# Kernel tuning notes

Measured on AMD Instinct MI355X. Metric: run time of the kernel, lower is better.

The kernel has to match this reference:

```python
import jax, jax.numpy as jnp
import numpy as np

D_MODEL, D_FFN, N_LEVELS, N_HEADS, N_POINTS = 256, 1024, 4, 8, 4
B, LQ = 2, 8192
SHAPES = [(128, 128), (64, 64), (32, 32), (16, 16)]  # (H_l, W_l) per level
D_HEAD = D_MODEL // N_HEADS


def setup_inputs() -> dict:
    key = jax.random.key(0)
    ks = jax.random.split(key, 16)
    S = sum(h * w for h, w in SHAPES)

    def lin_w(k, fin, fout):
        s = 1.0 / np.sqrt(fin)
        return jax.random.uniform(k, (fin, fout), jnp.float32, -s, s)

    inp = {
        "tgt": jax.random.normal(ks[0], (B, LQ, D_MODEL), jnp.float32),
        "query_pos": jax.random.normal(ks[1], (B, LQ, D_MODEL), jnp.float32),
        "reference_points": jax.random.uniform(ks[2], (B, LQ, N_LEVELS, 2), jnp.float32),
        "src": jax.random.normal(ks[3], (B, S, D_MODEL), jnp.float32),
        "spatial_shapes": np.array(SHAPES, dtype=np.int64),
        "level_start_index": np.concatenate([[0], np.cumsum([h * w for h, w in SHAPES])[:-1]]).astype(np.int64),
        "W_value": lin_w(ks[4], D_MODEL, D_MODEL),
        "b_value": jnp.zeros((D_MODEL,), jnp.float32),
        "W_off": lin_w(ks[5], D_MODEL, N_HEADS * N_LEVELS * N_POINTS * 2),
        "b_off": 0.5 * jax.random.normal(ks[6], (N_HEADS * N_LEVELS * N_POINTS * 2,), jnp.float32),
        "W_attn": lin_w(ks[7], D_MODEL, N_HEADS * N_LEVELS * N_POINTS),
        "b_attn": jnp.zeros((N_HEADS * N_LEVELS * N_POINTS,), jnp.float32),
        "W_out": lin_w(ks[8], D_MODEL, D_MODEL),
        "b_out": jnp.zeros((D_MODEL,), jnp.float32),
        "ln1_g": jnp.ones((D_MODEL,), jnp.float32),
        "ln1_b": jnp.zeros((D_MODEL,), jnp.float32),
        "W1": lin_w(ks[9], D_MODEL, D_FFN),
        "b1": jnp.zeros((D_FFN,), jnp.float32),
        "W2": lin_w(ks[10], D_FFN, D_MODEL),
        "b2": jnp.zeros((D_MODEL,), jnp.float32),
        "ln3_g": jnp.ones((D_MODEL,), jnp.float32),
        "ln3_b": jnp.zeros((D_MODEL,), jnp.float32),
    }
    return inp


def _layer_norm(x, g, b, eps=1e-5):
    mu = jnp.mean(x, -1, keepdims=True)
    var = jnp.mean((x - mu) ** 2, -1, keepdims=True)
    return (x - mu) * jax.lax.rsqrt(var + eps) * g + b


def _ms_deform_attn(q, reference_points, src, shapes,
                    W_value, b_value, W_off, b_off, W_attn, b_attn, W_out, b_out):
    Bq, Lq, _ = q.shape
    value = (src @ W_value + b_value).reshape(Bq, -1, N_HEADS, D_HEAD)
    value = jnp.transpose(value, (0, 2, 1, 3))  # [B, H, S, Dh]
    off = (q @ W_off + b_off).reshape(Bq, Lq, N_HEADS, N_LEVELS, N_POINTS, 2)
    attn = jax.nn.softmax((q @ W_attn + b_attn).reshape(Bq, Lq, N_HEADS, N_LEVELS * N_POINTS), axis=-1)
    attn = attn.reshape(Bq, Lq, N_HEADS, N_LEVELS, N_POINTS)
    # offset normalizer is (W_l, H_l) per level
    normalizer = jnp.array([[w, h] for h, w in shapes], jnp.float32)
    loc = reference_points[:, :, None, :, None, :] + off / normalizer[None, None, None, :, None, :]

    out = jnp.zeros((Bq, Lq, N_HEADS, D_HEAD), jnp.float32)
    start = 0
    for l, (Hl, Wl) in enumerate(shapes):
        Nl = Hl * Wl
        v_l = value[:, :, start:start + Nl]  # [B, H, Nl, Dh]
        start += Nl
        loc_l = jnp.transpose(loc[:, :, :, l, :, :], (0, 2, 1, 3, 4))  # [B, H, Lq, P, 2]
        # grid_sample (align_corners=False, zero padding) pixel coords
        x = loc_l[..., 0] * Wl - 0.5
        y = loc_l[..., 1] * Hl - 0.5
        x0, y0 = jnp.floor(x), jnp.floor(y)
        wx, wy = x - x0, y - y0
        acc = jnp.zeros((Bq, N_HEADS, Lq, N_POINTS, D_HEAD), jnp.float32)
        for dx, dy, w in ((0, 0, (1 - wx) * (1 - wy)), (1, 0, wx * (1 - wy)),
                          (0, 1, (1 - wx) * wy), (1, 1, wx * wy)):
            xi, yi = x0 + dx, y0 + dy
            valid = (xi >= 0) & (xi < Wl) & (yi >= 0) & (yi < Hl)
            idx = (jnp.clip(yi, 0, Hl - 1) * Wl + jnp.clip(xi, 0, Wl - 1)).astype(jnp.int32)
            g = jnp.take_along_axis(v_l, idx.reshape(Bq, N_HEADS, -1, 1), axis=2)
            g = g.reshape(Bq, N_HEADS, Lq, N_POINTS, D_HEAD)
            acc = acc + jnp.where(valid[..., None], w[..., None] * g, 0.0)
        a = jnp.transpose(attn[:, :, :, l, :], (0, 2, 1, 3))  # [B, H, Lq, P]
        out = out + jnp.einsum('bhqp,bhqpd->bqhd', a, acc)
    return out.reshape(Bq, Lq, D_MODEL) @ W_out + b_out


def reference(tgt, query_pos, reference_points, src, spatial_shapes, level_start_index,
              W_value, b_value, W_off, b_off, W_attn, b_attn, W_out, b_out,
              ln1_g, ln1_b, W1, b1, W2, b2, ln3_g, ln3_b):
    shapes = [(int(h), int(w)) for h, w in np.asarray(spatial_shapes)]
    q = tgt + query_pos  # with_pos_embed
    tgt2 = _ms_deform_attn(q, reference_points, src, shapes,
                           W_value, b_value, W_off, b_off, W_attn, b_attn, W_out, b_out)
    x = _layer_norm(tgt + tgt2, ln1_g, ln1_b)  # dropout = identity (eval)
    ff = jax.nn.relu(x @ W1 + b1) @ W2 + b2
    return _layer_norm(x + ff, ln3_g, ln3_b)
```

## Files before the change

### kernel.cpp

```cpp
#include <hip/hip_runtime.h>
#include <hip/hip_bf16.h>
#include <hip/hip_fp16.h>
#include <math.h>

#define D_MODEL   256
#define D_FFN     1024
#define N_LEVELS  4
#define N_HEADS   8
#define N_POINTS  4
#define BATCH     2
#define LQ        8192
#define S_TOTAL   21760
#define M_Q       (BATCH*LQ)
#define M_V       (BATCH*S_TOTAL)
#define VTILES    (M_V/128)

typedef __attribute__((ext_vector_type(8))) short bf16x8;
typedef __attribute__((ext_vector_type(4))) float floatx4;

struct alignas(8)  bh4 { __hip_bfloat16 a, b, c, d; };
struct alignas(16) bh8 { __hip_bfloat16 v[8]; };

__device__ __forceinline__ void gld_lds16(const void* g, void* l) {
    __builtin_amdgcn_global_load_lds(
        (const __attribute__((address_space(1))) void*)g,
        (__attribute__((address_space(3))) void*)l, 16, 0, 0);
}

template<int BM, int BN, int K>
__device__ __forceinline__ void gemm_core(const __hip_bfloat16* __restrict__ A,
                                          const __hip_bfloat16* __restrict__ Bt,
                                          int row0, int nb0, int lda, int ldb,
                                          short* As, short* Bs,
                                          floatx4 (&acc)[BM/64][BN/16])
{
    constexpr int NT  = BN / 16;
    constexpr int AF  = BM / 64;
    constexpr int BCH = BN / 64;
    constexpr int NIT = K / 32;

    const int tid  = threadIdx.x;
    const int w    = tid >> 6;
    const int lane = tid & 63;
    const int quad = lane >> 4;
    const int l15  = lane & 15;
    const size_t ldaB = (size_t)lda * 2, ldbB = (size_t)ldb * 2;

    const char* gA[AF]; int lA[AF];
#pragma unroll
    for (int i = 0; i < AF; i++) {
        int o = (w * AF + i) * 1024 + lane * 16;
        gA[i] = (const char*)A + (size_t)(row0 + (o >> 6)) * ldaB + (o & 63);
        lA[i] = (w * AF + i) * 512;
    }
    const char* gB[BCH]; int lB[BCH];
#pragma unroll
    for (int j = 0; j < BCH; j++) {
        int o = (w * BCH + j) * 1024 + lane * 16;
        gB[j] = (const char*)Bt + (size_t)(nb0 + (o >> 6)) * ldbB + (o & 63);
        lB[j] = (w * BCH + j) * 512;
    }

#pragma unroll
    for (int i = 0; i < AF; i++)  gld_lds16(gA[i], &As[lA[i]]);
#pragma unroll
    for (int j = 0; j < BCH; j++) gld_lds16(gB[j], &Bs[lB[j]]);

#pragma unroll 8
    for (int it = 0; it < NIT; ++it) {
        __syncthreads();
        const int cb = it & 1;
        if (it + 1 < NIT) {
            const size_t kb = (size_t)(it + 1) * 64;
            const int nb = cb ^ 1;
#pragma unroll
            for (int i = 0; i < AF; i++)  gld_lds16(gA[i] + kb, &As[nb * BM * 32 + lA[i]]);
#pragma unroll
            for (int j = 0; j < BCH; j++) gld_lds16(gB[j] + kb, &Bs[nb * BN * 32 + lB[j]]);
        }
        const short* Ab = &As[cb * BM * 32];
        const short* Bb = &Bs[cb * BN * 32];
        bf16x8 af[AF];
#pragma unroll
        for (int mi = 0; mi < AF; mi++)
            af[mi] = *(const bf16x8*)&Ab[(w * (AF * 16) + mi * 16 + l15) * 32 + quad * 8];
#pragma unroll
        for (int ni = 0; ni < NT; ni++) {
            bf16x8 bfr = *(const bf16x8*)&Bb[(ni * 16 + l15) * 32 + quad * 8];
#pragma unroll
            for (int mi = 0; mi < AF; mi++)
                acc[mi][ni] = __builtin_amdgcn_mfma_f32_16x16x32_bf16(af[mi], bfr, acc[mi][ni], 0, 0, 0);
        }
    }
}

template<int BM, int BN, int K, int EPI>
__global__ __launch_bounds__(256)
void mfma_gemm(const __hip_bfloat16* __restrict__ A,
               const __hip_bfloat16* __restrict__ Bt,
               const float* __restrict__ bias,
               float* __restrict__ outf, __hip_bfloat16* __restrict__ outb,
               int lda, int ldb, int ldOut, long zStride)
{
    constexpr int NT = BN / 16, AF = BM / 64;
    __shared__ alignas(16) short As[2 * BM * 32];
    __shared__ alignas(16) short Bs[2 * BN * 32];

    const int tid = threadIdx.x, w = tid >> 6, lane = tid & 63;
    const int quad = lane >> 4, l15 = lane & 15;
    const int row0 = blockIdx.x * BM, nb0 = blockIdx.y * BN;
    const int z = blockIdx.z;

    floatx4 acc[AF][NT];
#pragma unroll
    for (int mi = 0; mi < AF; mi++)
#pragma unroll
        for (int ni = 0; ni < NT; ni++) acc[mi][ni] = (floatx4){0.f, 0.f, 0.f, 0.f};

    gemm_core<BM, BN, K>(A + (size_t)z * K, Bt + (size_t)z * K,
                         row0, nb0, lda, ldb, As, Bs, acc);

    float bias_c[NT];
#pragma unroll
    for (int ni = 0; ni < NT; ni++) bias_c[ni] = bias ? bias[nb0 + ni * 16 + l15] : 0.f;

    float* of = outf + (size_t)z * zStride;
#pragma unroll
    for (int mi = 0; mi < AF; mi++)
#pragma unroll
        for (int r = 0; r < 4; r++) {
            int row = row0 + w * (AF * 16) + mi * 16 + quad * 4 + r;
            size_t rb = (size_t)row * ldOut + nb0;
#pragma unroll
            for (int ni = 0; ni < NT; ni++) {
                float v = acc[mi][ni][r] + bias_c[ni];
                if (EPI == 2) outb[rb + ni * 16 + l15] = __float2bfloat16(fmaxf(v, 0.f));
                else          of[rb + ni * 16 + l15] = v;
            }
        }
}

__global__ __launch_bounds__(256)
void mfma_gemm_vq(const __hip_bfloat16* __restrict__ srcb,
                  const __hip_bfloat16* __restrict__ Wvt,
                  const float* __restrict__ b_value,
                  __hip_bfloat16* __restrict__ valueb,
                  const __hip_bfloat16* __restrict__ qb,
                  const __hip_bfloat16* __restrict__ Woat,
                  const float* __restrict__ b_off, const float* __restrict__ b_attn,
                  float* __restrict__ offb, float* __restrict__ attnb)
{
    __shared__ alignas(16) short As[2 * 128 * 32];
    __shared__ alignas(16) short Bs[2 * 128 * 32];

    const bool isV = blockIdx.x < VTILES;
    if (isV && blockIdx.y == 2) return;

    const int tid = threadIdx.x, w = tid >> 6, lane = tid & 63;
    const int quad = lane >> 4, l15 = lane & 15;
    const int nb0 = blockIdx.y * 128;

    floatx4 acc[2][8];
#pragma unroll
    for (int mi = 0; mi < 2; mi++)
#pragma unroll
        for (int ni = 0; ni < 8; ni++) acc[mi][ni] = (floatx4){0.f, 0.f, 0.f, 0.f};

    if (isV) {
        const int row0 = blockIdx.x * 128;
        gemm_core<128, 128, 256>(srcb, Wvt, row0, nb0, 256, 256, As, Bs, acc);
        float bias_c[8];
#pragma unroll
        for (int ni = 0; ni < 8; ni++) bias_c[ni] = b_value[nb0 + ni * 16 + l15];
#pragma unroll
        for (int mi = 0; mi < 2; mi++)
#pragma unroll
            for (int r = 0; r < 4; r++) {
                int row = row0 + w * 32 + mi * 16 + quad * 4 + r;
                size_t rb = (size_t)row * 256 + nb0;
#pragma unroll
                for (int ni = 0; ni < 8; ni++)
                    valueb[rb + ni * 16 + l15] = __float2bfloat16(acc[mi][ni][r] + bias_c[ni]);
            }
        return;
    }

    const int row0 = (blockIdx.x - VTILES) * 128;
    gemm_core<128, 128, 256>(qb, Woat, row0, nb0, 256, 256, As, Bs, acc);

    if (blockIdx.y < 2) {
        float bias_c[8];
#pragma unroll
        for (int ni = 0; ni < 8; ni++) bias_c[ni] = b_off[nb0 + ni * 16 + l15];
#pragma unroll
        for (int mi = 0; mi < 2; mi++)
#pragma unroll
            for (int r = 0; r < 4; r++) {
                int row = row0 + w * 32 + mi * 16 + quad * 4 + r;
                size_t rb = (size_t)row * 256 + nb0;
#pragma unroll
                for (int ni = 0; ni < 8; ni++)
                    offb[rb + ni * 16 + l15] = acc[mi][ni][r] + bias_c[ni];
            }
    } else {
        float bias_c[8];
#pragma unroll
        for (int ni = 0; ni < 8; ni++) bias_c[ni] = b_attn[ni * 16 + l15];
#pragma unroll
        for (int mi = 0; mi < 2; mi++)
#pragma unroll
            for (int r = 0; r < 4; r++) {
                int row = row0 + w * 32 + mi * 16 + quad * 4 + r;
                size_t rb = (size_t)row * 128;
#pragma unroll
                for (int ni = 0; ni < 8; ni++) {
                    float v = acc[mi][ni][r] + bias_c[ni];
                    float m = v;
#pragma unroll
                    for (int msk = 1; msk <= 8; msk <<= 1) m = fmaxf(m, __shfl_xor(m, msk));
                    float e = __expf(v - m);
                    float ssum = e;
#pragma unroll
                    for (int msk = 1; msk <= 8; msk <<= 1) ssum += __shfl_xor(ssum, msk);
                    attnb[rb + ni * 16 + l15] = e / ssum;
                }
            }
    }
}

__global__ __launch_bounds__(256)
void ln_kernel(const float* __restrict__ in1, const float* __restrict__ in2,
               const float* __restrict__ resid, const float* __restrict__ bias,
               const float* __restrict__ g, const float* __restrict__ b,
               float* __restrict__ outf, __hip_bfloat16* __restrict__ outb)
{
    const int row  = blockIdx.x * 4 + (threadIdx.x >> 6);
    const int lane = threadIdx.x & 63;
    const size_t rb = (size_t)row * 256 + lane * 4;

    float4 v = *(const float4*)(resid + rb);
    float4 a = *(const float4*)(in1 + rb);
    v.x += a.x; v.y += a.y; v.z += a.z; v.w += a.w;
    if (in2) {
        float4 c = *(const float4*)(in2 + rb);
        v.x += c.x; v.y += c.y; v.z += c.z; v.w += c.w;
    }
    if (bias) {
        float4 c = *(const float4*)(bias + lane * 4);
        v.x += c.x; v.y += c.y; v.z += c.z; v.w += c.w;
    }
    float s  = v.x + v.y + v.z + v.w;
    float sq = v.x * v.x + v.y * v.y + v.z * v.z + v.w * v.w;
#pragma unroll
    for (int msk = 1; msk <= 32; msk <<= 1) {
        s += __shfl_xor(s, msk); sq += __shfl_xor(sq, msk);
    }
    float mean = s * (1.f / 256.f);
    float var  = sq * (1.f / 256.f) - mean * mean;
    float rstd = rsqrtf(var + 1e-5f);
    float4 gg = *(const float4*)(g + lane * 4);
    float4 bb = *(const float4*)(b + lane * 4);
    float4 o;
    o.x = (v.x - mean) * rstd * gg.x + bb.x;
    o.y = (v.y - mean) * rstd * gg.y + bb.y;
    o.z = (v.z - mean) * rstd * gg.z + bb.z;
    o.w = (v.w - mean) * rstd * gg.w + bb.w;
    *(float4*)(outf + rb) = o;
    if (outb)
        *(bh4*)(outb + rb) = { __float2bfloat16(o.x), __float2bfloat16(o.y),
                               __float2bfloat16(o.z), __float2bfloat16(o.w) };
}

__global__ __launch_bounds__(256)
void prep_kernel(const float* w0, const float* w1, const float* w2,
                 const float* w3, const float* w4, const float* w5,
                 __hip_bfloat16* o0, __hip_bfloat16* o1, __hip_bfloat16* o2,
                 __hip_bfloat16* o3, __hip_bfloat16* o4, __hip_bfloat16* o5,
                 const float* src, __hip_bfloat16* srcb,
                 const float* tgt, const float* qpos, __hip_bfloat16* qb)
{
    const int bx = blockIdx.x;
    if (bx < 736) {
        int t = bx;
        const float* s; __hip_bfloat16* dst; int Kd, Nd, tl;
        if      (t < 64)  { s = w0; dst = o0; Kd = 256;  Nd = 256;  tl = t; }
        else if (t < 128) { s = w1; dst = o1; Kd = 256;  Nd = 256;  tl = t - 64; }
        else if (t < 160) { s = w2; dst = o2; Kd = 256;  Nd = 128;  tl = t - 128; }
        else if (t < 224) { s = w3; dst = o3; Kd = 256;  Nd = 256;  tl = t - 160; }
        else if (t < 480) { s = w4; dst = o4; Kd = 256;  Nd = 1024; tl = t - 224; }
        else              { s = w5; dst = o5; Kd = 1024; Nd = 256;  tl = t - 480; }
        int ntn = Nd >> 5;
        int kt = tl / ntn, nt = tl - kt * ntn;
        __shared__ float T[32][33];
        int tx = threadIdx.x & 31, ty = threadIdx.x >> 5;
#pragma unroll
        for (int i = 0; i < 4; i++) {
            int k = kt * 32 + ty + i * 8;
            T[tx][ty + i * 8] = s[(size_t)k * Nd + nt * 32 + tx];
        }
        __syncthreads();
#pragma unroll
        for (int i = 0; i < 4; i++) {
            int n = nt * 32 + ty + i * 8;
            dst[(size_t)n * Kd + kt * 32 + tx] = __float2bfloat16(T[ty + i * 8][tx]);
        }
    } else if (bx < 736 + 10880) {
        int i = (bx - 736) * 256 + threadIdx.x;
        float4 v = ((const float4*)src)[i];
        ((bh4*)srcb)[i] = { __float2bfloat16(v.x), __float2bfloat16(v.y),
                            __float2bfloat16(v.z), __float2bfloat16(v.w) };
    } else {
        int i = (bx - 736 - 10880) * 256 + threadIdx.x;
        float4 x = ((const float4*)tgt)[i];
        float4 y = ((const float4*)qpos)[i];
        ((bh4*)qb)[i] = { __float2bfloat16(x.x + y.x), __float2bfloat16(x.y + y.y),
                          __float2bfloat16(x.z + y.z), __float2bfloat16(x.w + y.w) };
    }
}

#define QB 8
__global__ __launch_bounds__(256)
void sample_kernel(const float* __restrict__ refp, const float* __restrict__ offb,
                   const float* __restrict__ attn,
                   const __hip_bfloat16* __restrict__ value,
                   __hip_bfloat16* __restrict__ tgt2)
{
    __shared__ unsigned spk[64 * 65];

    const int q0  = blockIdx.x * QB;
    const int tid = threadIdx.x;

#pragma unroll
    for (int k = 0; k < 4; k++) {
        const int it = tid + k * 256;
        const int ql = it >> 7, h = (it >> 4) & 7, lp = it & 15;
        const int l = lp >> 2, p = lp & 3;
        const int q = q0 + ql, b = q >> 13;
        const int Wl = 128 >> l;
        const int LST = (l == 0) ? 0 : (l == 1) ? 16384 : (l == 2) ? 20480 : 21504;

        const float rx = refp[((size_t)q * N_LEVELS + l) * 2 + 0];
        const float ry = refp[((size_t)q * N_LEVELS + l) * 2 + 1];
        const float ox = offb[(size_t)q * 256 + h * 32 + l * 8 + p * 2 + 0];
        const float oy = offb[(size_t)q * 256 + h * 32 + l * 8 + p * 2 + 1];
        const float a  = attn[(size_t)q * 128 + h * 16 + lp];

        const float x = rx * Wl - 0.5f + ox;
        const float y = ry * Wl - 0.5f + oy;
        const float x0f = floorf(x), y0f = floorf(y);
        const float wx = x - x0f, wy = y - y0f;
        const int ix = (int)x0f, iy = (int)y0f;
        const int base = b * S_TOTAL + LST;
        const int g = ql * 8 + h;
        const float cw[4] = {(1.f - wx) * (1.f - wy) * a, wx * (1.f - wy) * a,
                             (1.f - wx) * wy * a,         wx * wy * a};
#pragma unroll
        for (int c = 0; c < 4; c++) {
            const int xi = ix + (c & 1), yi = iy + (c >> 1);
            const bool valid = ((unsigned)xi < (unsigned)Wl) && ((unsigned)yi < (unsigned)Wl);
            const unsigned pix = valid ? (unsigned)(base + yi * Wl + xi) : (unsigned)base;
            const __half hw = __float2half(valid ? cw[c] : 0.f);
            spk[(lp * 4 + c) * 65 + g] = (pix << 16) | (unsigned)__half_as_ushort(hw);
        }
    }
    __syncthreads();

    const int ql = tid >> 5, h = (tid >> 2) & 7, d4 = tid & 3;
    const int q = q0 + ql, g = ql * 8 + h;
    const int c0 = h * 32 + d4 * 8;
    const char* vb = (const char*)value + (size_t)c0 * 2;

    float ac[8] = {0.f, 0.f, 0.f, 0.f, 0.f, 0.f, 0.f, 0.f};
#pragma unroll
    for (int sc = 0; sc < 64; sc++) {
        unsigned u = spk[sc * 65 + g];
        float wv = __half2float(__ushort_as_half((unsigned short)(u & 0xffffu)));
        uint4 rv = *(const uint4*)(vb + ((size_t)(u >> 16) << 9));
        ac[0] += wv * __uint_as_float(rv.x << 16);
        ac[1] += wv * __uint_as_float(rv.x & 0xffff0000u);
        ac[2] += wv * __uint_as_float(rv.y << 16);
        ac[3] += wv * __uint_as_float(rv.y & 0xffff0000u);
        ac[4] += wv * __uint_as_float(rv.z << 16);
        ac[5] += wv * __uint_as_float(rv.z & 0xffff0000u);
        ac[6] += wv * __uint_as_float(rv.w << 16);
        ac[7] += wv * __uint_as_float(rv.w & 0xffff0000u);
    }
    bh8 o;
#pragma unroll
    for (int i = 0; i < 8; i++) o.v[i] = __float2bfloat16(ac[i]);
    *(bh8*)(tgt2 + (size_t)q * 256 + c0) = o;
}

extern "C" void kernel_launch(void* const* d_in, const int* in_sizes, int n_in,
                              void* d_out, int out_size, void* d_ws, size_t ws_size,
                              hipStream_t stream) {
    const float* tgt     = (const float*)d_in[0];
    const float* qpos    = (const float*)d_in[1];
    const float* refp    = (const float*)d_in[2];
    const float* src     = (const float*)d_in[3];
    const float* W_value = (const float*)d_in[6];
    const float* b_value = (const float*)d_in[7];
    const float* W_off   = (const float*)d_in[8];
    const float* b_off   = (const float*)d_in[9];
    const float* W_attn  = (const float*)d_in[10];
    const float* b_attn  = (const float*)d_in[11];
    const float* W_out   = (const float*)d_in[12];
    const float* b_out   = (const float*)d_in[13];
    const float* ln1_g   = (const float*)d_in[14];
    const float* ln1_b   = (const float*)d_in[15];
    const float* W1      = (const float*)d_in[16];
    const float* b1      = (const float*)d_in[17];
    const float* W2      = (const float*)d_in[18];
    const float* b2      = (const float*)d_in[19];
    const float* ln3_g   = (const float*)d_in[20];
    const float* ln3_b   = (const float*)d_in[21];
    float* out = (float*)d_out;

    char* p = (char*)d_ws;
    auto nxt = [&](size_t b) { char* r = p; p += (b + 255) & ~(size_t)255; return r; };
    __hip_bfloat16* Wvt    = (__hip_bfloat16*)nxt((size_t)256 * 256 * 2);
    __hip_bfloat16* Woat   = (__hip_bfloat16*)nxt((size_t)384 * 256 * 2);
    __hip_bfloat16* Woutt  = (__hip_bfloat16*)nxt((size_t)256 * 256 * 2);
    __hip_bfloat16* W1t    = (__hip_bfloat16*)nxt((size_t)1024 * 256 * 2);
    __hip_bfloat16* W2t    = (__hip_bfloat16*)nxt((size_t)256 * 1024 * 2);
    __hip_bfloat16* srcb   = (__hip_bfloat16*)nxt((size_t)M_V * 256 * 2);
    __hip_bfloat16* qb     = (__hip_bfloat16*)nxt((size_t)M_Q * 256 * 2);
    __hip_bfloat16* valueb = (__hip_bfloat16*)nxt((size_t)M_V * 256 * 2);
    float*          offb   = (float*)nxt((size_t)M_Q * 256 * 4);
    float*          attnb  = (float*)nxt((size_t)M_Q * 128 * 4);
    __hip_bfloat16* tgt2b  = (__hip_bfloat16*)nxt((size_t)M_Q * 256 * 2);
    float*          x      = (float*)nxt((size_t)M_Q * 256 * 4);
    __hip_bfloat16* xb     = (__hip_bfloat16*)nxt((size_t)M_Q * 256 * 2);
    __hip_bfloat16* hb     = (__hip_bfloat16*)nxt((size_t)M_Q * 1024 * 2);
    float* t2o = offb;
    float* p0  = (float*)srcb;
    float* p1  = p0 + (size_t)M_Q * 256;

    dim3 blk(256);

    prep_kernel<<<dim3(736 + 10880 + 4096), blk, 0, stream>>>(
        W_value, W_off, W_attn, W_out, W1, W2,
        Wvt, Woat, Woat + 256 * 256, Woutt, W1t, W2t,
        src, srcb, tgt, qpos, qb);

    mfma_gemm_vq<<<dim3(VTILES + M_Q / 128, 3), blk, 0, stream>>>(
        srcb, Wvt, b_value, valueb, qb, Woat, b_off, b_attn, offb, attnb);

    sample_kernel<<<dim3(M_Q / QB), blk, 0, stream>>>(refp, offb, attnb, valueb, tgt2b);

    mfma_gemm<64, 128, 256, 0><<<dim3(M_Q / 64, 2), blk, 0, stream>>>(
        tgt2b, Woutt, b_out, t2o, nullptr, 256, 256, 256, 0);

    ln_kernel<<<dim3(M_Q / 4), blk, 0, stream>>>(
        t2o, nullptr, tgt, nullptr, ln1_g, ln1_b, x, xb);

    mfma_gemm<128, 128, 256, 2><<<dim3(M_Q / 128, 8), blk, 0, stream>>>(
        xb, W1t, b1, nullptr, hb, 256, 256, 1024, 0);

    mfma_gemm<64, 128, 512, 0><<<dim3(M_Q / 64, 2, 2), blk, 0, stream>>>(
        hb, W2t, nullptr, p0, nullptr, 1024, 1024, 256, (long)M_Q * 256);

    ln_kernel<<<dim3(M_Q / 4), blk, 0, stream>>>(
        p0, p1, x, b2, ln3_g, ln3_b, out, nullptr);
}
```

Baseline: 301.2 us.

## Fuse fp32-to-bf16 input conversion into value/query GEMM and batch sample gathers

The separate conversion pass over src and tgt+query_pos is removed. The value/offset GEMM now loads fp32 A tiles directly, adds query_pos in registers, packs to bf16 and writes them into LDS, which avoids a full write and re-read of the bf16 copies. The output projection now stores bf16 that the first layernorm reads, and the sampling loop issues 16 gathers at a time with an occupancy hint to raise memory-level parallelism. In exchange, A tiles are staged through registers rather than async global-to-LDS loads, and the output projection result is rounded to bf16 before the residual add.

```diff
diff --git a/kernel.cpp b/kernel.cpp
--- a/kernel.cpp
+++ b/kernel.cpp
@@ -27,6 +27,15 @@
         (__attribute__((address_space(3))) void*)l, 16, 0, 0);
 }
 
+__device__ __forceinline__ bh8 pack8(float4 a, float4 b) {
+    bh8 o;
+    o.v[0] = __float2bfloat16(a.x); o.v[1] = __float2bfloat16(a.y);
+    o.v[2] = __float2bfloat16(a.z); o.v[3] = __float2bfloat16(a.w);
+    o.v[4] = __float2bfloat16(b.x); o.v[5] = __float2bfloat16(b.y);
+    o.v[6] = __float2bfloat16(b.z); o.v[7] = __float2bfloat16(b.w);
+    return o;
+}
+
 template<int BM, int BN, int K>
 __device__ __forceinline__ void gemm_core(const __hip_bfloat16* __restrict__ A,
                                           const __hip_bfloat16* __restrict__ Bt,
@@ -94,6 +103,87 @@
     }
 }
 
+template<int K, bool ADD>
+__device__ __forceinline__ void gemm_core_cvtA(const float* __restrict__ Af,
+                                               const float* __restrict__ A2f,
+                                               const __hip_bfloat16* __restrict__ Bt,
+                                               int row0, int nb0, int lda, int ldb,
+                                               short* As, short* Bs,
+                                               floatx4 (&acc)[2][8])
+{
+    constexpr int NIT = K / 32;
+    const int tid  = threadIdx.x;
+    const int w    = tid >> 6;
+    const int lane = tid & 63;
+    const int quad = lane >> 4;
+    const int l15  = lane & 15;
+
+    const int arow = tid >> 1, akb = (tid & 1) * 16;
+    const float* gA  = Af + (size_t)(row0 + arow) * lda + akb;
+    const float* gA2 = ADD ? (A2f + (size_t)(row0 + arow) * lda + akb) : nullptr;
+    const int aoff = arow * 32 + akb;
+
+    const size_t ldbB = (size_t)ldb * 2;
+    const char* gB[2]; int lB[2];
+#pragma unroll
+    for (int j = 0; j < 2; j++) {
+        int o = (w * 2 + j) * 1024 + lane * 16;
+        gB[j] = (const char*)Bt + (size_t)(nb0 + (o >> 6)) * ldbB + (o & 63);
+        lB[j] = (w * 2 + j) * 512;
+    }
+
+    float4 fv[4];
+#pragma unroll
+    for (int i = 0; i < 4; i++) {
+        fv[i] = *(const float4*)(gA + i * 4);
+        if (ADD) {
+            float4 t = *(const float4*)(gA2 + i * 4);
+            fv[i].x += t.x; fv[i].y += t.y; fv[i].z += t.z; fv[i].w += t.w;
+        }
+    }
+#pragma unroll
+    for (int j = 0; j < 2; j++) gld_lds16(gB[j], &Bs[lB[j]]);
+    *(bh8*)&As[aoff]     = pack8(fv[0], fv[1]);
+    *(bh8*)&As[aoff + 8] = pack8(fv[2], fv[3]);
+
+#pragma unroll 8
+    for (int it = 0; it < NIT; ++it) {
+        __syncthreads();
+        const int cb = it & 1;
+        const bool more = (it + 1 < NIT);
+        if (more) {
+            const int kt = (it + 1) * 32;
+#pragma unroll
+            for (int i = 0; i < 4; i++) {
+                fv[i] = *(const float4*)(gA + kt + i * 4);
+                if (ADD) {
+                    float4 t = *(const float4*)(gA2 + kt + i * 4);
+                    fv[i].x += t.x; fv[i].y += t.y; fv[i].z += t.z; fv[i].w += t.w;
+                }
+            }
+#pragma unroll
+            for (int j = 0; j < 2; j++)
+                gld_lds16(gB[j] + (size_t)(it + 1) * 64, &Bs[(cb ^ 1) * 128 * 32 + lB[j]]);
+        }
+        const short* Ab = &As[cb * 128 * 32];
+        const short* Bb = &Bs[cb * 128 * 32];
+        bf16x8 af[2];
+        af[0] = *(const bf16x8*)&Ab[(w * 32      + l15) * 32 + quad * 8];
+        af[1] = *(const bf16x8*)&Ab[(w * 32 + 16 + l15) * 32 + quad * 8];
+#pragma unroll
+        for (int ni = 0; ni < 8; ni++) {
+            bf16x8 bfr = *(const bf16x8*)&Bb[(ni * 16 + l15) * 32 + quad * 8];
+            acc[0][ni] = __builtin_amdgcn_mfma_f32_16x16x32_bf16(af[0], bfr, acc[0][ni], 0, 0, 0);
+            acc[1][ni] = __builtin_amdgcn_mfma_f32_16x16x32_bf16(af[1], bfr, acc[1][ni], 0, 0, 0);
+        }
+        if (more) {
+            short* dst = &As[(cb ^ 1) * 128 * 32 + aoff];
+            *(bh8*)dst       = pack8(fv[0], fv[1]);
+            *(bh8*)(dst + 8) = pack8(fv[2], fv[3]);
+        }
+    }
+}
+
 template<int BM, int BN, int K, int EPI>
 __global__ __launch_bounds__(256)
 void mfma_gemm(const __hip_bfloat16* __restrict__ A,
@@ -134,18 +224,19 @@
 #pragma unroll
             for (int ni = 0; ni < NT; ni++) {
                 float v = acc[mi][ni][r] + bias_c[ni];
-                if (EPI == 2) outb[rb + ni * 16 + l15] = __float2bfloat16(fmaxf(v, 0.f));
-                else          of[rb + ni * 16 + l15] = v;
+                if (EPI == 2)      outb[rb + ni * 16 + l15] = __float2bfloat16(fmaxf(v, 0.f));
+                else if (EPI == 1) outb[rb + ni * 16 + l15] = __float2bfloat16(v);
+                else               of[rb + ni * 16 + l15] = v;
             }
         }
 }
 
 __global__ __launch_bounds__(256)
-void mfma_gemm_vq(const __hip_bfloat16* __restrict__ srcb,
+void mfma_gemm_vq(const float* __restrict__ src,
                   const __hip_bfloat16* __restrict__ Wvt,
                   const float* __restrict__ b_value,
                   __hip_bfloat16* __restrict__ valueb,
-                  const __hip_bfloat16* __restrict__ qb,
+                  const float* __restrict__ tgt, const float* __restrict__ qpos,
                   const __hip_bfloat16* __restrict__ Woat,
                   const float* __restrict__ b_off, const float* __restrict__ b_attn,
                   float* __restrict__ offb, float* __restrict__ attnb)
@@ -168,7 +259,7 @@
 
     if (isV) {
         const int row0 = blockIdx.x * 128;
-        gemm_core<128, 128, 256>(srcb, Wvt, row0, nb0, 256, 256, As, Bs, acc);
+        gemm_core_cvtA<256, false>(src, nullptr, Wvt, row0, nb0, 256, 256, As, Bs, acc);
         float bias_c[8];
 #pragma unroll
         for (int ni = 0; ni < 8; ni++) bias_c[ni] = b_value[nb0 + ni * 16 + l15];
@@ -186,7 +277,7 @@
     }
 
     const int row0 = (blockIdx.x - VTILES) * 128;
-    gemm_core<128, 128, 256>(qb, Woat, row0, nb0, 256, 256, As, Bs, acc);
+    gemm_core_cvtA<256, true>(tgt, qpos, Woat, row0, nb0, 256, 256, As, Bs, acc);
 
     if (blockIdx.y < 2) {
         float bias_c[8];
@@ -228,8 +319,10 @@
     }
 }
 
+template<bool B1>
 __global__ __launch_bounds__(256)
-void ln_kernel(const float* __restrict__ in1, const float* __restrict__ in2,
+void ln_kernel(const float* __restrict__ in1f, const __hip_bfloat16* __restrict__ in1b,
+               const float* __restrict__ in2,
                const float* __restrict__ resid, const float* __restrict__ bias,
                const float* __restrict__ g, const float* __restrict__ b,
                float* __restrict__ outf, __hip_bfloat16* __restrict__ outb)
@@ -239,8 +332,14 @@
     const size_t rb = (size_t)row * 256 + lane * 4;
 
     float4 v = *(const float4*)(resid + rb);
-    float4 a = *(const float4*)(in1 + rb);
-    v.x += a.x; v.y += a.y; v.z += a.z; v.w += a.w;
+    if (B1) {
+        bh4 a = *(const bh4*)(in1b + rb);
+        v.x += __bfloat162float(a.a); v.y += __bfloat162float(a.b);
+        v.z += __bfloat162float(a.c); v.w += __bfloat162float(a.d);
+    } else {
+        float4 a = *(const float4*)(in1f + rb);
+        v.x += a.x; v.y += a.y; v.z += a.z; v.w += a.w;
+    }
     if (in2) {
         float4 c = *(const float4*)(in2 + rb);
         v.x += c.x; v.y += c.y; v.z += c.z; v.w += c.w;
@@ -275,51 +374,35 @@
 void prep_kernel(const float* w0, const float* w1, const float* w2,
                  const float* w3, const float* w4, const float* w5,
                  __hip_bfloat16* o0, __hip_bfloat16* o1, __hip_bfloat16* o2,
-                 __hip_bfloat16* o3, __hip_bfloat16* o4, __hip_bfloat16* o5,
-                 const float* src, __hip_bfloat16* srcb,
-                 const float* tgt, const float* qpos, __hip_bfloat16* qb)
-{
-    const int bx = blockIdx.x;
-    if (bx < 736) {
-        int t = bx;
-        const float* s; __hip_bfloat16* dst; int Kd, Nd, tl;
-        if      (t < 64)  { s = w0; dst = o0; Kd = 256;  Nd = 256;  tl = t; }
-        else if (t < 128) { s = w1; dst = o1; Kd = 256;  Nd = 256;  tl = t - 64; }
-        else if (t < 160) { s = w2; dst = o2; Kd = 256;  Nd = 128;  tl = t - 128; }
-        else if (t < 224) { s = w3; dst = o3; Kd = 256;  Nd = 256;  tl = t - 160; }
-        else if (t < 480) { s = w4; dst = o4; Kd = 256;  Nd = 1024; tl = t - 224; }
-        else              { s = w5; dst = o5; Kd = 1024; Nd = 256;  tl = t - 480; }
-        int ntn = Nd >> 5;
-        int kt = tl / ntn, nt = tl - kt * ntn;
-        __shared__ float T[32][33];
-        int tx = threadIdx.x & 31, ty = threadIdx.x >> 5;
-#pragma unroll
-        for (int i = 0; i < 4; i++) {
-            int k = kt * 32 + ty + i * 8;
-            T[tx][ty + i * 8] = s[(size_t)k * Nd + nt * 32 + tx];
-        }
-        __syncthreads();
-#pragma unroll
-        for (int i = 0; i < 4; i++) {
-            int n = nt * 32 + ty + i * 8;
-            dst[(size_t)n * Kd + kt * 32 + tx] = __float2bfloat16(T[ty + i * 8][tx]);
-        }
-    } else if (bx < 736 + 10880) {
-        int i = (bx - 736) * 256 + threadIdx.x;
-        float4 v = ((const float4*)src)[i];
-        ((bh4*)srcb)[i] = { __float2bfloat16(v.x), __float2bfloat16(v.y),
-                            __float2bfloat16(v.z), __float2bfloat16(v.w) };
-    } else {
-        int i = (bx - 736 - 10880) * 256 + threadIdx.x;
-        float4 x = ((const float4*)tgt)[i];
-        float4 y = ((const float4*)qpos)[i];
-        ((bh4*)qb)[i] = { __float2bfloat16(x.x + y.x), __float2bfloat16(x.y + y.y),
-                          __float2bfloat16(x.z + y.z), __float2bfloat16(x.w + y.w) };
+                 __hip_bfloat16* o3, __hip_bfloat16* o4, __hip_bfloat16* o5)
+{
+    int t = blockIdx.x;
+    const float* s; __hip_bfloat16* dst; int Kd, Nd, tl;
+    if      (t < 64)  { s = w0; dst = o0; Kd = 256;  Nd = 256;  tl = t; }
+    else if (t < 128) { s = w1; dst = o1; Kd = 256;  Nd = 256;  tl = t - 64; }
+    else if (t < 160) { s = w2; dst = o2; Kd = 256;  Nd = 128;  tl = t - 128; }
+    else if (t < 224) { s = w3; dst = o3; Kd = 256;  Nd = 256;  tl = t - 160; }
+    else if (t < 480) { s = w4; dst = o4; Kd = 256;  Nd = 1024; tl = t - 224; }
+    else              { s = w5; dst = o5; Kd = 1024; Nd = 256;  tl = t - 480; }
+    int ntn = Nd >> 5;
+    int kt = tl / ntn, nt = tl - kt * ntn;
+    __shared__ float T[32][33];
+    int tx = threadIdx.x & 31, ty = threadIdx.x >> 5;
+#pragma unroll
+    for (int i = 0; i < 4; i++) {
+        int k = kt * 32 + ty + i * 8;
+        T[tx][ty + i * 8] = s[(size_t)k * Nd + nt * 32 + tx];
+    }
+    __syncthreads();
+#pragma unroll
+    for (int i = 0; i < 4; i++) {
+        int n = nt * 32 + ty + i * 8;
+        dst[(size_t)n * Kd + kt * 32 + tx] = __float2bfloat16(T[ty + i * 8][tx]);
     }
 }
 
 #define QB 8
-__global__ __launch_bounds__(256)
+__global__ __launch_bounds__(256, 4)
 void sample_kernel(const float* __restrict__ refp, const float* __restrict__ offb,
                    const float* __restrict__ attn,
                    const __hip_bfloat16* __restrict__ value,
@@ -372,18 +455,26 @@
 
     float ac[8] = {0.f, 0.f, 0.f, 0.f, 0.f, 0.f, 0.f, 0.f};
 #pragma unroll
-    for (int sc = 0; sc < 64; sc++) {
-        unsigned u = spk[sc * 65 + g];
-        float wv = __half2float(__ushort_as_half((unsigned short)(u & 0xffffu)));
-        uint4 rv = *(const uint4*)(vb + ((size_t)(u >> 16) << 9));
-        ac[0] += wv * __uint_as_float(rv.x << 16);
-        ac[1] += wv * __uint_as_float(rv.x & 0xffff0000u);
-        ac[2] += wv * __uint_as_float(rv.y << 16);
-        ac[3] += wv * __uint_as_float(rv.y & 0xffff0000u);
-        ac[4] += wv * __uint_as_float(rv.z << 16);
-        ac[5] += wv * __uint_as_float(rv.z & 0xffff0000u);
-        ac[6] += wv * __uint_as_float(rv.w << 16);
-        ac[7] += wv * __uint_as_float(rv.w & 0xffff0000u);
+    for (int ch = 0; ch < 4; ch++) {
+        unsigned us[16];
+#pragma unroll
+        for (int j = 0; j < 16; j++) us[j] = spk[(ch * 16 + j) * 65 + g];
+        uint4 rv[16];
+#pragma unroll
+        for (int j = 0; j < 16; j++)
+            rv[j] = *(const uint4*)(vb + ((size_t)(us[j] >> 16) << 9));
+#pragma unroll
+        for (int j = 0; j < 16; j++) {
+            float wv = __half2float(__ushort_as_half((unsigned short)(us[j] & 0xffffu)));
+            ac[0] += wv * __uint_as_float(rv[j].x << 16);
+            ac[1] += wv * __uint_as_float(rv[j].x & 0xffff0000u);
+            ac[2] += wv * __uint_as_float(rv[j].y << 16);
+            ac[3] += wv * __uint_as_float(rv[j].y & 0xffff0000u);
+            ac[4] += wv * __uint_as_float(rv[j].z << 16);
+            ac[5] += wv * __uint_as_float(rv[j].z & 0xffff0000u);
+            ac[6] += wv * __uint_as_float(rv[j].w << 16);
+            ac[7] += wv * __uint_as_float(rv[j].w & 0xffff0000u);
+        }
     }
     bh8 o;
 #pragma unroll
@@ -423,36 +514,33 @@
     __hip_bfloat16* Woutt  = (__hip_bfloat16*)nxt((size_t)256 * 256 * 2);
     __hip_bfloat16* W1t    = (__hip_bfloat16*)nxt((size_t)1024 * 256 * 2);
     __hip_bfloat16* W2t    = (__hip_bfloat16*)nxt((size_t)256 * 1024 * 2);
-    __hip_bfloat16* srcb   = (__hip_bfloat16*)nxt((size_t)M_V * 256 * 2);
-    __hip_bfloat16* qb     = (__hip_bfloat16*)nxt((size_t)M_Q * 256 * 2);
     __hip_bfloat16* valueb = (__hip_bfloat16*)nxt((size_t)M_V * 256 * 2);
     float*          offb   = (float*)nxt((size_t)M_Q * 256 * 4);
     float*          attnb  = (float*)nxt((size_t)M_Q * 128 * 4);
     __hip_bfloat16* tgt2b  = (__hip_bfloat16*)nxt((size_t)M_Q * 256 * 2);
+    __hip_bfloat16* t2ob   = (__hip_bfloat16*)nxt((size_t)M_Q * 256 * 2);
     float*          x      = (float*)nxt((size_t)M_Q * 256 * 4);
     __hip_bfloat16* xb     = (__hip_bfloat16*)nxt((size_t)M_Q * 256 * 2);
     __hip_bfloat16* hb     = (__hip_bfloat16*)nxt((size_t)M_Q * 1024 * 2);
-    float* t2o = offb;
-    float* p0  = (float*)srcb;
-    float* p1  = p0 + (size_t)M_Q * 256;
+    float* p0 = (float*)valueb;
+    float* p1 = p0 + (size_t)M_Q * 256;
 
     dim3 blk(256);
 
-    prep_kernel<<<dim3(736 + 10880 + 4096), blk, 0, stream>>>(
+    prep_kernel<<<dim3(736), blk, 0, stream>>>(
         W_value, W_off, W_attn, W_out, W1, W2,
-        Wvt, Woat, Woat + 256 * 256, Woutt, W1t, W2t,
-        src, srcb, tgt, qpos, qb);
+        Wvt, Woat, Woat + 256 * 256, Woutt, W1t, W2t);
 
     mfma_gemm_vq<<<dim3(VTILES + M_Q / 128, 3), blk, 0, stream>>>(
-        srcb, Wvt, b_value, valueb, qb, Woat, b_off, b_attn, offb, attnb);
+        src, Wvt, b_value, valueb, tgt, qpos, Woat, b_off, b_attn, offb, attnb);
 
     sample_kernel<<<dim3(M_Q / QB), blk, 0, stream>>>(refp, offb, attnb, valueb, tgt2b);
 
-    mfma_gemm<64, 128, 256, 0><<<dim3(M_Q / 64, 2), blk, 0, stream>>>(
-        tgt2b, Woutt, b_out, t2o, nullptr, 256, 256, 256, 0);
-
-    ln_kernel<<<dim3(M_Q / 4), blk, 0, stream>>>(
-        t2o, nullptr, tgt, nullptr, ln1_g, ln1_b, x, xb);
+    mfma_gemm<64, 128, 256, 1><<<dim3(M_Q / 64, 2), blk, 0, stream>>>(
+        tgt2b, Woutt, b_out, nullptr, t2ob, 256, 256, 256, 0);
+
+    ln_kernel<true><<<dim3(M_Q / 4), blk, 0, stream>>>(
+        nullptr, t2ob, nullptr, tgt, nullptr, ln1_g, ln1_b, x, xb);
 
     mfma_gemm<128, 128, 256, 2><<<dim3(M_Q / 128, 8), blk, 0, stream>>>(
         xb, W1t, b1, nullptr, hb, 256, 256, 1024, 0);
@@ -460,6 +548,6 @@
     mfma_gemm<64, 128, 512, 0><<<dim3(M_Q / 64, 2, 2), blk, 0, stream>>>(
         hb, W2t, nullptr, p0, nullptr, 1024, 1024, 256, (long)M_Q * 256);
 
-    ln_kernel<<<dim3(M_Q / 4), blk, 0, stream>>>(
-        p0, p1, x, b2, ln3_g, ln3_b, out, nullptr);
-}
+    ln_kernel<false><<<dim3(M_Q / 4), blk, 0, stream>>>(
+        p0, nullptr, p1, x, b2, ln3_g, ln3_b, out, nullptr);
+}
```

Result: no change. 301.3 us (+0.0%).
